# Optimization experiments

Hardware: AMD Instinct MI355X
Metric: run time of the kernel (lower is better)

## Reference

```python
import jax, jax.numpy as jnp
import numpy as np
import math

D_MODEL = 512
DIM_K = 512
DIM_V = 512
N_HEADS = 8
B, S = 2, 2048


def setup_inputs() -> dict:
    key = jax.random.key(0)
    ks = jax.random.split(key, 10)
    s = 1.0 / math.sqrt(D_MODEL)
    return {
        "x": jax.random.normal(ks[0], (B, S, D_MODEL), jnp.float32),
        "y": jax.random.normal(ks[1], (B, S, D_MODEL), jnp.float32),
        # torch nn.Linear weights: [out, in]
        "q_w": jax.random.normal(ks[2], (DIM_K, D_MODEL), jnp.float32) * s,
        "q_b": jax.random.normal(ks[3], (DIM_K,), jnp.float32) * s,
        "k_w": jax.random.normal(ks[4], (DIM_K, D_MODEL), jnp.float32) * s,
        "k_b": jax.random.normal(ks[5], (DIM_K,), jnp.float32) * s,
        "v_w": jax.random.normal(ks[6], (DIM_V, D_MODEL), jnp.float32) * s,
        "v_b": jax.random.normal(ks[7], (DIM_V,), jnp.float32) * s,
        "o_w": jax.random.normal(ks[8], (D_MODEL, DIM_V), jnp.float32) * s,
        "o_b": jax.random.normal(ks[9], (D_MODEL,), jnp.float32) * s,
    }


def reference(x, y, q_w, q_b, k_w, k_b, v_w, v_b, o_w, o_b):
    b, s, _ = x.shape
    hd_k = DIM_K // N_HEADS
    hd_v = DIM_V // N_HEADS
    norm_fact = 1.0 / math.sqrt(D_MODEL)  # note: original scales by 1/sqrt(d_model)
    # torch code reshapes the flat [B,S,dim] projection row-major into [H,B,S,hd]
    Q = (x @ q_w.T + q_b).reshape(N_HEADS, b, s, hd_k)
    K = (y @ k_w.T + k_b).reshape(N_HEADS, b, s, hd_k)
    V = (y @ v_w.T + v_b).reshape(N_HEADS, b, s, hd_v)
    # scores: [H, B, Sq, Sk]
    scores = jnp.einsum("hbqd,hbkd->hbqk", Q, K) * norm_fact
    # per-row mean threshold: mask (set -inf) where score <= row mean
    thre = jnp.mean(scores, axis=-1, keepdims=True)
    scores = jnp.where(scores <= thre, -jnp.inf, scores)
    attn = jax.nn.softmax(scores, axis=-1)
    out = jnp.einsum("hbqk,hbkd->hbqd", attn, V).reshape(b, s, DIM_V)
    return out @ o_w.T + o_b
```

## Files before the change

kernel.cpp:

```cpp
#include <hip/hip_runtime.h>


typedef unsigned short ushort;
typedef unsigned int uint;

typedef __bf16  bf16x8   __attribute__((ext_vector_type(8)));
typedef float   floatx4  __attribute__((ext_vector_type(4)));
typedef float   floatx16 __attribute__((ext_vector_type(16)));
typedef float   float4v  __attribute__((ext_vector_type(4)));
typedef uint    uint4v   __attribute__((ext_vector_type(4)));
typedef ushort  ushort4v __attribute__((ext_vector_type(4)));

#define MFMA16(a,b,c) __builtin_amdgcn_mfma_f32_16x16x32_bf16((a),(b),(c),0,0,0)
#define MFMA32(a,b,c) __builtin_amdgcn_mfma_f32_32x32x16_bf16((a),(b),(c),0,0,0)

__device__ __forceinline__ float b2f(ushort u){
  union { uint i; float f; } v; v.i = ((uint)u) << 16; return v.f;
}
__device__ __forceinline__ ushort f2b(float f){
  union { float f; uint i; } v; v.f = f;
  uint r = v.i + 0x7FFFu + ((v.i >> 16) & 1u);
  return (ushort)(r >> 16);
}
__device__ __forceinline__ void split2(float f, ushort& h, ushort& l){
  h = f2b(f);
  l = f2b(f - b2f(h));
}
__device__ __forceinline__ void gload16(const ushort* g, ushort* l){
  __builtin_amdgcn_global_load_lds(
      (const __attribute__((address_space(1))) unsigned int*)g,
      (__attribute__((address_space(3))) unsigned int*)l, 16, 0, 0);
}

__global__ __launch_bounds__(256) void split_all(
    const float* __restrict__ x, const float* __restrict__ y,
    const float* __restrict__ qw, const float* __restrict__ kw,
    const float* __restrict__ vw, const float* __restrict__ ow,
    ushort* __restrict__ xhi, ushort* __restrict__ xlo,
    ushort* __restrict__ yhi, ushort* __restrict__ ylo,
    ushort* __restrict__ qwh, ushort* __restrict__ qwl,
    ushort* __restrict__ kwh, ushort* __restrict__ kwl,
    ushort* __restrict__ vwh, ushort* __restrict__ owh)
{
  int idx = blockIdx.x * 256 + threadIdx.x;
  if (idx < 1048576){
    const float* sp; ushort *hp, *lp; int i;
    if (idx < 524288){ sp = x; hp = xhi; lp = xlo; i = idx; }
    else             { sp = y; hp = yhi; lp = ylo; i = idx - 524288; }
    float4v d = ((const float4v*)sp)[i];
    ushort4v h, l;
    #pragma unroll
    for (int j=0;j<4;j++){ ushort hh,ll; split2(d[j],hh,ll); h[j]=hh; l[j]=ll; }
    ((ushort4v*)hp)[i] = h;
    ((ushort4v*)lp)[i] = l;
  } else {
    int k = idx - 1048576;
    int a = k >> 16, i = k & 65535;
    if (a < 2){
      const float* sp = a ? kw : qw;
      ushort *hp = a ? kwh : qwh, *lp = a ? kwl : qwl;
      float4v d = ((const float4v*)sp)[i];
      ushort4v h, l;
      #pragma unroll
      for (int j=0;j<4;j++){ ushort hh,ll; split2(d[j],hh,ll); h[j]=hh; l[j]=ll; }
      ((ushort4v*)hp)[i] = h;
      ((ushort4v*)lp)[i] = l;
    } else {
      const float* sp = (a == 2) ? vw : ow;
      ushort *hp = (a == 2) ? vwh : owh;
      float4v d = ((const float4v*)sp)[i];
      ushort4v h;
      #pragma unroll
      for (int j=0;j<4;j++) h[j] = f2b(d[j]);
      ((ushort4v*)hp)[i] = h;
    }
  }
}

__global__ __launch_bounds__(256) void proj_qkv(
    const ushort* __restrict__ xhi, const ushort* __restrict__ xlo,
    const ushort* __restrict__ yhi, const ushort* __restrict__ ylo,
    const ushort* __restrict__ qwh, const ushort* __restrict__ qwl,
    const ushort* __restrict__ kwh, const ushort* __restrict__ kwl,
    const ushort* __restrict__ vwh,
    const float* __restrict__ q_b, const float* __restrict__ k_b,
    const float* __restrict__ v_b,
    ushort* __restrict__ pq_hi, ushort* __restrict__ pq_lo,
    ushort* __restrict__ pk_hi, ushort* __restrict__ pk_lo,
    ushort* __restrict__ pv, float* __restrict__ ksum_out)
{
  const int seg = blockIdx.x >> 9;
  const int id  = blockIdx.x & 511;
  const int m0 = ((id & 7) * 8 + ((id >> 3) & 7)) * 64;
  const int n0 = (id >> 6) * 64;
  const bool split = (seg < 2);

  const ushort* Ahi = (seg == 0) ? xhi : yhi;
  const ushort* Alo = (seg == 0) ? xlo : ylo;
  const ushort* Bhi = (seg == 0) ? qwh : ((seg == 1) ? kwh : vwh);
  const ushort* Blo = (seg == 0) ? qwl : kwl;
  const float*  bias = (seg == 0) ? q_b : ((seg == 1) ? k_b : v_b);
  ushort* outhi = (seg == 0) ? pq_hi : ((seg == 1) ? pk_hi : pv);
  ushort* outlo = (seg == 0) ? pq_lo : pk_lo;

  __shared__ __align__(16) ushort AH[2][4096];
  __shared__ __align__(16) ushort AL[2][4096];
  __shared__ __align__(16) ushort BH[2][4096];
  __shared__ __align__(16) ushort BL[2][4096];
  __shared__ float cs[64];

  const int t    = threadIdx.x;
  const int lane = t & 63;
  const int w    = t >> 6;
  const int wm   = w >> 1, wn = w & 1;
  const int lr   = lane & 15, lg = lane >> 4;

  const int rl  = lane >> 3;
  const int c8s = (lane & 7) ^ rl;

  auto stage = [&](int buf, int k0){
    if (split){
      #pragma unroll
      for (int j = 0; j < 8; j++){
        const int c = w * 8 + j;
        if (c < 8)
          gload16(Ahi + (size_t)(m0 + c*8 + rl)*512 + k0 + c8s*8, &AH[buf][c*512]);
        else if (c < 16)
          gload16(Alo + (size_t)(m0 + (c-8)*8 + rl)*512 + k0 + c8s*8, &AL[buf][(c-8)*512]);
        else if (c < 24)
          gload16(Bhi + (size_t)(n0 + (c-16)*8 + rl)*512 + k0 + c8s*8, &BH[buf][(c-16)*512]);
        else
          gload16(Blo + (size_t)(n0 + (c-24)*8 + rl)*512 + k0 + c8s*8, &BL[buf][(c-24)*512]);
      }
    } else {
      #pragma unroll
      for (int j = 0; j < 4; j++){
        const int c = w * 4 + j;
        if (c < 8)
          gload16(Ahi + (size_t)(m0 + c*8 + rl)*512 + k0 + c8s*8, &AH[buf][c*512]);
        else
          gload16(Bhi + (size_t)(n0 + (c-8)*8 + rl)*512 + k0 + c8s*8, &BH[buf][(c-8)*512]);
      }
    }
  };

  floatx4 zf; zf[0]=0.f; zf[1]=0.f; zf[2]=0.f; zf[3]=0.f;
  floatx4 acc[2][2];
  #pragma unroll
  for (int i=0;i<2;i++)
    #pragma unroll
    for (int j=0;j<2;j++) acc[i][j] = zf;

  stage(0, 0);
  __syncthreads();

  int cur = 0;
  for (int it = 0; it < 8; ++it){
    if (it < 7) stage(cur^1, (it+1)*64);

    #pragma unroll
    for (int ks=0; ks<2; ks++){
      const int xo = ((ks*4 + lg) ^ (lr & 7)) << 3;
      bf16x8 ah[2], al[2], bh[2], bl[2];
      #pragma unroll
      for (int mi=0;mi<2;mi++){
        const int off = (wm*32 + mi*16 + lr)*64 + xo;
        ah[mi] = *(const bf16x8*)&AH[cur][off];
        if (split) al[mi] = *(const bf16x8*)&AL[cur][off];
      }
      #pragma unroll
      for (int ni=0;ni<2;ni++){
        const int off = (wn*32 + ni*16 + lr)*64 + xo;
        bh[ni] = *(const bf16x8*)&BH[cur][off];
        if (split) bl[ni] = *(const bf16x8*)&BL[cur][off];
      }
      #pragma unroll
      for (int mi=0;mi<2;mi++)
        #pragma unroll
        for (int ni=0;ni<2;ni++){
          acc[mi][ni] = MFMA16(ah[mi], bh[ni], acc[mi][ni]);
          if (split){
            acc[mi][ni] = MFMA16(ah[mi], bl[ni], acc[mi][ni]);
            acc[mi][ni] = MFMA16(al[mi], bh[ni], acc[mi][ni]);
          }
        }
    }
    __syncthreads();
    cur ^= 1;
  }

  #pragma unroll
  for (int ni=0;ni<2;ni++){
    const int n = n0 + wn*32 + ni*16 + lr;
    const float bn = bias[n];
    #pragma unroll
    for (int mi=0;mi<2;mi++){
      #pragma unroll
      for (int r=0;r<4;r++){
        const int m = m0 + wm*32 + mi*16 + lg*4 + r;
        const float c = acc[mi][ni][r] + bn;
        const size_t off = (size_t)m*512 + n;
        if (split){ ushort h,l; split2(c,h,l); outhi[off]=h; outlo[off]=l; }
        else      { outhi[off] = f2b(c); }
      }
    }
  }

  if (seg == 1) {
    if (t < 64) cs[t] = 0.f;
    __syncthreads();
    #pragma unroll
    for (int ni=0;ni<2;ni++){
      float s = 0.f;
      #pragma unroll
      for (int mi=0;mi<2;mi++)
        #pragma unroll
        for (int r=0;r<4;r++) s += acc[mi][ni][r];
      atomicAdd(&cs[wn*32 + ni*16 + lr], s);
    }
    __syncthreads();
    if (t < 64){
      const int hb = m0 >> 8;
      atomicAdd(&ksum_out[hb*64 + t], cs[t] + 64.f * bias[n0 + t]);
    }
  }
}

__global__ __launch_bounds__(256) void vtrans(
    const ushort* __restrict__ pv, ushort* __restrict__ vt)
{
  const int hb = blockIdx.y;
  const int s0 = blockIdx.x * 64;
  const size_t cb = (size_t)hb * 131072;
  __shared__ __align__(16) ushort T[64][68];
  const int t = threadIdx.x;
  {
    int s = t >> 2, c = (t & 3) * 16;
    *(uint4v*)&T[s][c]     = *(const uint4v*)&pv[cb + (size_t)(s0+s)*64 + c];
    *(uint4v*)&T[s][c + 8] = *(const uint4v*)&pv[cb + (size_t)(s0+s)*64 + c + 8];
  }
  __syncthreads();
  const int d = t >> 2, sc = (t & 3) * 16;
  ushort buf[16];
  #pragma unroll
  for (int i=0;i<16;i++) buf[i] = T[sc + i][d];
  *(uint4v*)&vt[cb + (size_t)d*2048 + s0 + sc]     = *(const uint4v*)&buf[0];
  *(uint4v*)&vt[cb + (size_t)d*2048 + s0 + sc + 8] = *(const uint4v*)&buf[8];
}

__device__ __forceinline__ void stage_kh(
    ushort* dst, const ushort* gk, size_t cb, int kvb, int ws, int l)
{
  const int rsub = l >> 3;
  const int c8   = (l & 7) ^ rsub;
  #pragma unroll
  for (int j = 0; j < 2; j++){
    const int sub = ws*2 + j;
    const int row = sub*8 + rsub;
    gload16(gk + cb + (size_t)(kvb + row)*64 + c8*8, dst + sub*512);
  }
}
__device__ __forceinline__ void stage_vt(
    ushort* dst, const ushort* gvt, size_t cb, int kvb, int ws, int l)
{
  const int rsub = l >> 3;
  const int c8   = (l & 7) ^ rsub;
  #pragma unroll
  for (int j = 0; j < 2; j++){
    const int sub = ws*2 + j;
    const int row = sub*8 + rsub;
    gload16(gvt + cb + (size_t)row*2048 + kvb + c8*8, dst + sub*512);
  }
}

__global__ __launch_bounds__(512) void attn_kernel(
    const ushort* __restrict__ qhi, const ushort* __restrict__ qlo,
    const ushort* __restrict__ khi, const ushort* __restrict__ klo,
    const ushort* __restrict__ vt,  const float* __restrict__ ksum,
    ushort* __restrict__ Oa, ushort* __restrict__ Ob,
    float* __restrict__ za, float* __restrict__ zb)
{
  const int id = blockIdx.x;
  const int hb = ((id & 7) << 1) | ((id >> 3) & 1);
  const int kv = (id >> 4) & 1;
  const int q0 = (id >> 5) * 128;
  const size_t cb = (size_t)hb * 131072;
  const float C1 = 0.04419417382415922f * 1.44269504088896f;

  __shared__ __align__(16) ushort SMEM[32768];

  const int t = threadIdx.x, l = t & 63, w = t >> 6;
  const int half = w >> 2, ws = w & 3;
  const int lq = l & 31, h = l >> 5;
  const int kbase = kv*1024 + half*512;

  ushort* op = kv ? Ob : Oa;
  float*  zp = kv ? zb : za;

  ushort* KH0 = SMEM + (half*2)*4096;
  ushort* KH1 = SMEM + (half*2+1)*4096;
  ushort* VTB = SMEM + 16384 + half*4096;
  ushort* KLB = SMEM + 24576 + half*4096;

  stage_kh(KH0, khi, cb, kbase, ws, l);
  stage_kh(KLB, klo, cb, kbase, ws, l);

  union U8 { bf16x8 v; ushort u[8]; };
  U8 qfh[4], qfl[4];
  float part = 0.f;
  #pragma unroll
  for (int st=0; st<4; st++){
    size_t g = cb + (size_t)(q0 + ws*32 + lq)*64 + st*16 + h*8;
    qfh[st].v = *(const bf16x8*)&qhi[g];
    qfl[st].v = *(const bf16x8*)&qlo[g];
    float4v k0 = *(const float4v*)&ksum[hb*64 + st*16 + h*8];
    float4v k1 = *(const float4v*)&ksum[hb*64 + st*16 + h*8 + 4];
    #pragma unroll
    for (int j=0;j<4;j++) part += (b2f(qfh[st].u[j])   + b2f(qfl[st].u[j]))   * k0[j];
    #pragma unroll
    for (int j=0;j<4;j++) part += (b2f(qfh[st].u[4+j]) + b2f(qfl[st].u[4+j])) * k1[j];
  }
  part += __shfl_xor(part, 32);
  const float rm = part * (1.f/2048.f);
  const float nrmc = -rm * C1;

  floatx16 O0 = {0,0,0,0,0,0,0,0,0,0,0,0,0,0,0,0};
  floatx16 O1 = O0;
  float za_r = 0.f, zb_r = 0.f;

  __syncthreads();

  for (int kt = 0; kt < 8; kt++){
    ushort* KHc = (kt & 1) ? KH1 : KH0;
    ushort* KHn = (kt & 1) ? KH0 : KH1;
    if (kt + 1 < 8) stage_kh(KHn, khi, cb, kbase + (kt+1)*64, ws, l);
    stage_vt(VTB, vt, cb, kbase + kt*64, ws, l);

    floatx16 s0 = {0,0,0,0,0,0,0,0,0,0,0,0,0,0,0,0};
    floatx16 s1 = s0;
    #pragma unroll
    for (int st=0; st<4; st++){
      const int xo = (((st*2 + h) ^ (lq & 7)) << 3);
      bf16x8 kh0 = *(const bf16x8*)&KHc[(lq     )*64 + xo];
      bf16x8 kl0 = *(const bf16x8*)&KLB[(lq     )*64 + xo];
      bf16x8 kh1 = *(const bf16x8*)&KHc[(32 + lq)*64 + xo];
      bf16x8 kl1 = *(const bf16x8*)&KLB[(32 + lq)*64 + xo];
      s0 = MFMA32(kh0, qfh[st].v, s0);
      s1 = MFMA32(kh1, qfh[st].v, s1);
      s0 = MFMA32(kh0, qfl[st].v, s0);
      s1 = MFMA32(kh1, qfl[st].v, s1);
      s0 = MFMA32(kl0, qfh[st].v, s0);
      s1 = MFMA32(kl1, qfh[st].v, s1);
    }
    __syncthreads();
    if (kt + 1 < 8) stage_kh(KLB, klo, cb, kbase + (kt+1)*64, ws, l);

    #pragma unroll
    for (int r=0;r<16;r++){
      float t0 = __builtin_fmaf(s0[r], C1, nrmc);
      float t1 = __builtin_fmaf(s1[r], C1, nrmc);
      float e0 = __builtin_amdgcn_exp2f(t0);
      float e1 = __builtin_amdgcn_exp2f(t1);
      e0 = (t0 > 0.f) ? e0 : 0.f;
      e1 = (t1 > 0.f) ? e1 : 0.f;
      za_r += e0; zb_r += e1;
      s0[r] = e0; s1[r] = e1;
    }

    bf16x8 pa[4];
    #pragma unroll
    for (int g=0; g<2; g++){
      const floatx16& sp = g ? s1 : s0;
      #pragma unroll
      for (int sg=0; sg<2; sg++){
        uint X0,X1,X2,X3;
        asm("v_cvt_pk_bf16_f32 %0, %1, %2" : "=v"(X0) : "v"(sp[sg*8+0]), "v"(sp[sg*8+1]));
        asm("v_cvt_pk_bf16_f32 %0, %1, %2" : "=v"(X1) : "v"(sp[sg*8+2]), "v"(sp[sg*8+3]));
        asm("v_cvt_pk_bf16_f32 %0, %1, %2" : "=v"(X2) : "v"(sp[sg*8+4]), "v"(sp[sg*8+5]));
        asm("v_cvt_pk_bf16_f32 %0, %1, %2" : "=v"(X3) : "v"(sp[sg*8+6]), "v"(sp[sg*8+7]));
        asm("v_permlane32_swap_b32 %0, %1" : "+v"(X0), "+v"(X2));
        asm("v_permlane32_swap_b32 %0, %1" : "+v"(X1), "+v"(X3));
        union { uint u[4]; bf16x8 v; } pu;
        pu.u[0]=X0; pu.u[1]=X1; pu.u[2]=X2; pu.u[3]=X3;
        pa[g*2+sg] = pu.v;
      }
    }

    #pragma unroll
    for (int s4=0; s4<4; s4++){
      const int xo = (((s4*2 + h) ^ (lq & 7)) << 3);
      bf16x8 vf0 = *(const bf16x8*)&VTB[(lq     )*64 + xo];
      bf16x8 vf1 = *(const bf16x8*)&VTB[(32 + lq)*64 + xo];
      O0 = MFMA32(pa[s4], vf0, O0);
      O1 = MFMA32(pa[s4], vf1, O1);
    }

    __syncthreads();
  }

  float zacc = za_r + zb_r;
  zacc += __shfl_xor(zacc, 32);
  float* CB = (float*)SMEM;
  const int ci = (ws*64 + l)*34;
  if (half == 1){
    #pragma unroll
    for (int i=0;i<16;i++){ CB[ci+i] = O0[i]; CB[ci+16+i] = O1[i]; }
    CB[ci+32] = zacc;
  }
  __syncthreads();
  if (half == 0){
    const float zsum = zacc + CB[ci+32];
    if (h == 0) zp[hb*2048 + q0 + ws*32 + l] = zsum;
    #pragma unroll
    for (int r=0;r<16;r++){ O0[r] += CB[ci+r]; O1[r] += CB[ci+16+r]; }
    #pragma unroll
    for (int r=0;r<16;r++){
      const int crow = (r&3) + ((r>>2)<<3) + (h<<2);
      const int q = q0 + ws*32 + crow;
      const size_t base = cb + (size_t)q*64 + lq;
      op[base]      = f2b(O0[r]);
      op[base + 32] = f2b(O1[r]);
    }
  }
}

__global__ __launch_bounds__(256) void proj_out(
    const ushort* __restrict__ Oa, const ushort* __restrict__ Ob,
    const float* __restrict__ za, const float* __restrict__ zb,
    const ushort* __restrict__ owh, const float* __restrict__ o_b,
    float* __restrict__ outf)
{
  const int id = blockIdx.x;
  const int m0 = ((id & 7) * 8 + ((id >> 3) & 7)) * 64;
  const int n0 = (id >> 6) * 64;

  __shared__ __align__(16) ushort AH[2][4096];
  __shared__ __align__(16) ushort BH[2][4096];

  const int t    = threadIdx.x;
  const int lane = t & 63;
  const int w    = t >> 6;
  const int wm   = w >> 1, wn = w & 1;
  const int lr   = lane & 15, lg = lane >> 4;

  const int rl  = lane >> 3;
  const int c8s = (lane & 7) ^ rl;

  auto stageB = [&](int buf, int k0){
    #pragma unroll
    for (int j = 0; j < 2; j++){
      const int c = w*2 + j;
      gload16(owh + (size_t)(n0 + c*8 + rl)*512 + k0 + c8s*8, &BH[buf][c*512]);
    }
  };

  const int ar = t >> 2, ac = t & 3;
  uint4v la0, la1, lb0, lb1;
  auto issueA = [&](int k0){
    const size_t base = (size_t)(m0 + ar)*512 + k0 + ac*16;
    la0 = *(const uint4v*)&Oa[base];
    la1 = *(const uint4v*)&Oa[base + 8];
    lb0 = *(const uint4v*)&Ob[base];
    lb1 = *(const uint4v*)&Ob[base + 8];
  };
  auto writeA = [&](int buf, int k0){
    const int m = m0 + ar;
    const int zq = (m >> 8)*2048 + (m & 255)*8 + (k0 >> 6);
    const float zi = 1.f / (za[zq] + zb[zq]);
    uint4v o0, o1;
    #pragma unroll
    for (int j=0;j<4;j++){
      float l0 = (b2f((ushort)(la0[j] & 0xffff)) + b2f((ushort)(lb0[j] & 0xffff))) * zi;
      float h0 = (b2f((ushort)(la0[j] >> 16))    + b2f((ushort)(lb0[j] >> 16)))    * zi;
      o0[j] = (uint)f2b(l0) | ((uint)f2b(h0) << 16);
      float l1 = (b2f((ushort)(la1[j] & 0xffff)) + b2f((ushort)(lb1[j] & 0xffff))) * zi;
      float h1 = (b2f((ushort)(la1[j] >> 16))    + b2f((ushort)(lb1[j] >> 16)))    * zi;
      o1[j] = (uint)f2b(l1) | ((uint)f2b(h1) << 16);
    }
    const int p0 = ar*64 + (((ac*2    ) ^ (ar & 7)) << 3);
    const int p1 = ar*64 + (((ac*2 + 1) ^ (ar & 7)) << 3);
    *(uint4v*)&AH[buf][p0] = o0;
    *(uint4v*)&AH[buf][p1] = o1;
  };

  floatx4 zf; zf[0]=0.f; zf[1]=0.f; zf[2]=0.f; zf[3]=0.f;
  floatx4 acc[2][2];
  #pragma unroll
  for (int i=0;i<2;i++)
    #pragma unroll
    for (int j=0;j<2;j++) acc[i][j] = zf;

  issueA(0);
  stageB(0, 0);
  writeA(0, 0);
  __syncthreads();

  int cur = 0;
  for (int it = 0; it < 8; ++it){
    if (it < 7){ issueA((it+1)*64); stageB(cur^1, (it+1)*64); }

    #pragma unroll
    for (int ks=0; ks<2; ks++){
      const int xo = ((ks*4 + lg) ^ (lr & 7)) << 3;
      bf16x8 ah[2], bh[2];
      #pragma unroll
      for (int mi=0;mi<2;mi++)
        ah[mi] = *(const bf16x8*)&AH[cur][(wm*32 + mi*16 + lr)*64 + xo];
      #pragma unroll
      for (int ni=0;ni<2;ni++)
        bh[ni] = *(const bf16x8*)&BH[cur][(wn*32 + ni*16 + lr)*64 + xo];
      #pragma unroll
      for (int mi=0;mi<2;mi++)
        #pragma unroll
        for (int ni=0;ni<2;ni++)
          acc[mi][ni] = MFMA16(ah[mi], bh[ni], acc[mi][ni]);
    }
    if (it < 7) writeA(cur^1, (it+1)*64);
    __syncthreads();
    cur ^= 1;
  }

  #pragma unroll
  for (int ni=0;ni<2;ni++){
    const int n = n0 + wn*32 + ni*16 + lr;
    const float bn = o_b[n];
    #pragma unroll
    for (int mi=0;mi<2;mi++){
      #pragma unroll
      for (int r=0;r<4;r++){
        const int m = m0 + wm*32 + mi*16 + lg*4 + r;
        outf[(size_t)m*512 + n] = acc[mi][ni][r] + bn;
      }
    }
  }
}

extern "C" void kernel_launch(void* const* d_in, const int* in_sizes, int n_in,
                              void* d_out, int out_size, void* d_ws, size_t ws_size,
                              hipStream_t stream)
{
  const float* x   = (const float*)d_in[0];
  const float* y   = (const float*)d_in[1];
  const float* q_w = (const float*)d_in[2];
  const float* q_b = (const float*)d_in[3];
  const float* k_w = (const float*)d_in[4];
  const float* k_b = (const float*)d_in[5];
  const float* v_w = (const float*)d_in[6];
  const float* v_b = (const float*)d_in[7];
  const float* o_w = (const float*)d_in[8];
  const float* o_b = (const float*)d_in[9];

  const size_t NE = 4096ull * 512;
  const size_t WN = 512ull * 512;
  ushort* p = (ushort*)d_ws;
  ushort* pq_hi = p;
  ushort* pq_lo = pq_hi + NE;
  ushort* pk_hi = pq_lo + NE;
  ushort* pk_lo = pk_hi + NE;
  ushort* pv    = pk_lo + NE;
  ushort* xhi   = pv + NE;
  ushort* xlo   = xhi + NE;
  ushort* yhi   = xlo + NE;
  ushort* ylo   = yhi + NE;
  ushort* vtg   = xhi;
  ushort* Oa    = pv;
  ushort* Ob    = yhi;
  float*  za    = (float*)ylo;
  float*  zb    = za + 32768;
  ushort* qwh = ylo + NE;
  ushort* qwl = qwh + WN;
  ushort* kwh = qwl + WN;
  ushort* kwl = kwh + WN;
  ushort* vwh = kwl + WN;
  ushort* owh = vwh + WN;
  float*  ksumb = (float*)(owh + WN);

  hipMemsetAsync(ksumb, 0, 16 * 64 * sizeof(float), stream);

  split_all<<<5120, 256, 0, stream>>>(x, y, q_w, k_w, v_w, o_w,
                                      xhi, xlo, yhi, ylo,
                                      qwh, qwl, kwh, kwl, vwh, owh);
  proj_qkv<<<1536, 256, 0, stream>>>(xhi, xlo, yhi, ylo,
                                     qwh, qwl, kwh, kwl, vwh,
                                     q_b, k_b, v_b,
                                     pq_hi, pq_lo, pk_hi, pk_lo, pv, ksumb);
  vtrans<<<dim3(32,16), 256, 0, stream>>>(pv, vtg);
  attn_kernel<<<512, 512, 0, stream>>>(pq_hi, pq_lo, pk_hi, pk_lo, vtg, ksumb,
                                       Oa, Ob, za, zb);
  proj_out<<<512, 256, 0, stream>>>(Oa, Ob, za, zb, owh, o_b, (float*)d_out);
}
```

Baseline: 107.3 us.

## Split attention KV range four ways across smaller blocks and reduce in proj_out

The attention kernel now launches 1024 blocks of 256 threads, each handling a quarter of the key range, instead of 512 blocks of 512 threads that merged two KV halves in shared memory. The in-block shared-memory reduction goes away and proj_out instead sums four partial O and z buffers. MFMA sections are wrapped in s_setprio to favour matrix issue. This is meant to raise occupancy and remove the intra-block reduction and barrier, at the cost of twice as many bf16 partials written to global memory and more loads in proj_out. Workspace layout is reorganised to fit the four partial buffers.

```diff
diff --git a/kernel.cpp b/kernel.cpp
--- a/kernel.cpp
+++ b/kernel.cpp
@@ -249,68 +249,65 @@
 }
 
 __device__ __forceinline__ void stage_kh(
-    ushort* dst, const ushort* gk, size_t cb, int kvb, int ws, int l)
+    ushort* dst, const ushort* gk, size_t cb, int kvb, int w, int l)
 {
   const int rsub = l >> 3;
   const int c8   = (l & 7) ^ rsub;
   #pragma unroll
   for (int j = 0; j < 2; j++){
-    const int sub = ws*2 + j;
+    const int sub = w*2 + j;
     const int row = sub*8 + rsub;
     gload16(gk + cb + (size_t)(kvb + row)*64 + c8*8, dst + sub*512);
   }
 }
 __device__ __forceinline__ void stage_vt(
-    ushort* dst, const ushort* gvt, size_t cb, int kvb, int ws, int l)
+    ushort* dst, const ushort* gvt, size_t cb, int kvb, int w, int l)
 {
   const int rsub = l >> 3;
   const int c8   = (l & 7) ^ rsub;
   #pragma unroll
   for (int j = 0; j < 2; j++){
-    const int sub = ws*2 + j;
+    const int sub = w*2 + j;
     const int row = sub*8 + rsub;
     gload16(gvt + cb + (size_t)row*2048 + kvb + c8*8, dst + sub*512);
   }
 }
 
-__global__ __launch_bounds__(512) void attn_kernel(
+__global__ __launch_bounds__(256) void attn_kernel(
     const ushort* __restrict__ qhi, const ushort* __restrict__ qlo,
     const ushort* __restrict__ khi, const ushort* __restrict__ klo,
     const ushort* __restrict__ vt,  const float* __restrict__ ksum,
-    ushort* __restrict__ Oa, ushort* __restrict__ Ob,
-    float* __restrict__ za, float* __restrict__ zb)
+    ushort* __restrict__ Obase, float* __restrict__ zbase)
 {
   const int id = blockIdx.x;
   const int hb = ((id & 7) << 1) | ((id >> 3) & 1);
-  const int kv = (id >> 4) & 1;
-  const int q0 = (id >> 5) * 128;
+  const int kv = (id >> 4) & 3;
+  const int q0 = (id >> 6) * 128;
   const size_t cb = (size_t)hb * 131072;
   const float C1 = 0.04419417382415922f * 1.44269504088896f;
 
-  __shared__ __align__(16) ushort SMEM[32768];
+  __shared__ __align__(16) ushort SMEM[16384];
+  ushort* KH0 = SMEM;
+  ushort* KH1 = SMEM + 4096;
+  ushort* VTB = SMEM + 8192;
+  ushort* KLB = SMEM + 12288;
 
   const int t = threadIdx.x, l = t & 63, w = t >> 6;
-  const int half = w >> 2, ws = w & 3;
   const int lq = l & 31, h = l >> 5;
-  const int kbase = kv*1024 + half*512;
-
-  ushort* op = kv ? Ob : Oa;
-  float*  zp = kv ? zb : za;
-
-  ushort* KH0 = SMEM + (half*2)*4096;
-  ushort* KH1 = SMEM + (half*2+1)*4096;
-  ushort* VTB = SMEM + 16384 + half*4096;
-  ushort* KLB = SMEM + 24576 + half*4096;
-
-  stage_kh(KH0, khi, cb, kbase, ws, l);
-  stage_kh(KLB, klo, cb, kbase, ws, l);
+  const int kbase = kv * 512;
+
+  ushort* op = Obase + (size_t)kv * 2097152;
+  float*  zp = zbase + kv * 32768;
+
+  stage_kh(KH0, khi, cb, kbase, w, l);
+  stage_kh(KLB, klo, cb, kbase, w, l);
 
   union U8 { bf16x8 v; ushort u[8]; };
   U8 qfh[4], qfl[4];
   float part = 0.f;
   #pragma unroll
   for (int st=0; st<4; st++){
-    size_t g = cb + (size_t)(q0 + ws*32 + lq)*64 + st*16 + h*8;
+    size_t g = cb + (size_t)(q0 + w*32 + lq)*64 + st*16 + h*8;
     qfh[st].v = *(const bf16x8*)&qhi[g];
     qfl[st].v = *(const bf16x8*)&qlo[g];
     float4v k0 = *(const float4v*)&ksum[hb*64 + st*16 + h*8];
@@ -333,11 +330,12 @@
   for (int kt = 0; kt < 8; kt++){
     ushort* KHc = (kt & 1) ? KH1 : KH0;
     ushort* KHn = (kt & 1) ? KH0 : KH1;
-    if (kt + 1 < 8) stage_kh(KHn, khi, cb, kbase + (kt+1)*64, ws, l);
-    stage_vt(VTB, vt, cb, kbase + kt*64, ws, l);
+    if (kt + 1 < 8) stage_kh(KHn, khi, cb, kbase + (kt+1)*64, w, l);
+    stage_vt(VTB, vt, cb, kbase + kt*64, w, l);
 
     floatx16 s0 = {0,0,0,0,0,0,0,0,0,0,0,0,0,0,0,0};
     floatx16 s1 = s0;
+    __builtin_amdgcn_s_setprio(1);
     #pragma unroll
     for (int st=0; st<4; st++){
       const int xo = (((st*2 + h) ^ (lq & 7)) << 3);
@@ -352,8 +350,9 @@
       s0 = MFMA32(kl0, qfh[st].v, s0);
       s1 = MFMA32(kl1, qfh[st].v, s1);
     }
+    __builtin_amdgcn_s_setprio(0);
     __syncthreads();
-    if (kt + 1 < 8) stage_kh(KLB, klo, cb, kbase + (kt+1)*64, ws, l);
+    if (kt + 1 < 8) stage_kh(KLB, klo, cb, kbase + (kt+1)*64, w, l);
 
     #pragma unroll
     for (int r=0;r<16;r++){
@@ -386,6 +385,7 @@
       }
     }
 
+    __builtin_amdgcn_s_setprio(1);
     #pragma unroll
     for (int s4=0; s4<4; s4++){
       const int xo = (((s4*2 + h) ^ (lq & 7)) << 3);
@@ -394,39 +394,26 @@
       O0 = MFMA32(pa[s4], vf0, O0);
       O1 = MFMA32(pa[s4], vf1, O1);
     }
+    __builtin_amdgcn_s_setprio(0);
 
     __syncthreads();
   }
 
   float zacc = za_r + zb_r;
   zacc += __shfl_xor(zacc, 32);
-  float* CB = (float*)SMEM;
-  const int ci = (ws*64 + l)*34;
-  if (half == 1){
-    #pragma unroll
-    for (int i=0;i<16;i++){ CB[ci+i] = O0[i]; CB[ci+16+i] = O1[i]; }
-    CB[ci+32] = zacc;
-  }
-  __syncthreads();
-  if (half == 0){
-    const float zsum = zacc + CB[ci+32];
-    if (h == 0) zp[hb*2048 + q0 + ws*32 + l] = zsum;
-    #pragma unroll
-    for (int r=0;r<16;r++){ O0[r] += CB[ci+r]; O1[r] += CB[ci+16+r]; }
-    #pragma unroll
-    for (int r=0;r<16;r++){
-      const int crow = (r&3) + ((r>>2)<<3) + (h<<2);
-      const int q = q0 + ws*32 + crow;
-      const size_t base = cb + (size_t)q*64 + lq;
-      op[base]      = f2b(O0[r]);
-      op[base + 32] = f2b(O1[r]);
-    }
+  if (h == 0) zp[hb*2048 + q0 + w*32 + l] = zacc;
+  #pragma unroll
+  for (int r=0;r<16;r++){
+    const int crow = (r&3) + ((r>>2)<<3) + (h<<2);
+    const int q = q0 + w*32 + crow;
+    const size_t base = cb + (size_t)q*64 + lq;
+    op[base]      = f2b(O0[r]);
+    op[base + 32] = f2b(O1[r]);
   }
 }
 
 __global__ __launch_bounds__(256) void proj_out(
-    const ushort* __restrict__ Oa, const ushort* __restrict__ Ob,
-    const float* __restrict__ za, const float* __restrict__ zb,
+    const ushort* __restrict__ Obase, const float* __restrict__ zbase,
     const ushort* __restrict__ owh, const float* __restrict__ o_b,
     float* __restrict__ outf)
 {
@@ -455,27 +442,35 @@
   };
 
   const int ar = t >> 2, ac = t & 3;
-  uint4v la0, la1, lb0, lb1;
+  uint4v la[4][2];
   auto issueA = [&](int k0){
     const size_t base = (size_t)(m0 + ar)*512 + k0 + ac*16;
-    la0 = *(const uint4v*)&Oa[base];
-    la1 = *(const uint4v*)&Oa[base + 8];
-    lb0 = *(const uint4v*)&Ob[base];
-    lb1 = *(const uint4v*)&Ob[base + 8];
+    #pragma unroll
+    for (int p2=0;p2<4;p2++){
+      la[p2][0] = *(const uint4v*)&Obase[(size_t)p2*2097152 + base];
+      la[p2][1] = *(const uint4v*)&Obase[(size_t)p2*2097152 + base + 8];
+    }
   };
   auto writeA = [&](int buf, int k0){
     const int m = m0 + ar;
     const int zq = (m >> 8)*2048 + (m & 255)*8 + (k0 >> 6);
-    const float zi = 1.f / (za[zq] + zb[zq]);
+    float zs = 0.f;
+    #pragma unroll
+    for (int p2=0;p2<4;p2++) zs += zbase[p2*32768 + zq];
+    const float zi = 1.f / zs;
     uint4v o0, o1;
     #pragma unroll
     for (int j=0;j<4;j++){
-      float l0 = (b2f((ushort)(la0[j] & 0xffff)) + b2f((ushort)(lb0[j] & 0xffff))) * zi;
-      float h0 = (b2f((ushort)(la0[j] >> 16))    + b2f((ushort)(lb0[j] >> 16)))    * zi;
-      o0[j] = (uint)f2b(l0) | ((uint)f2b(h0) << 16);
-      float l1 = (b2f((ushort)(la1[j] & 0xffff)) + b2f((ushort)(lb1[j] & 0xffff))) * zi;
-      float h1 = (b2f((ushort)(la1[j] >> 16))    + b2f((ushort)(lb1[j] >> 16)))    * zi;
-      o1[j] = (uint)f2b(l1) | ((uint)f2b(h1) << 16);
+      float lo0=0.f, hi0=0.f, lo1=0.f, hi1=0.f;
+      #pragma unroll
+      for (int p2=0;p2<4;p2++){
+        lo0 += b2f((ushort)(la[p2][0][j] & 0xffff));
+        hi0 += b2f((ushort)(la[p2][0][j] >> 16));
+        lo1 += b2f((ushort)(la[p2][1][j] & 0xffff));
+        hi1 += b2f((ushort)(la[p2][1][j] >> 16));
+      }
+      o0[j] = (uint)f2b(lo0*zi) | ((uint)f2b(hi0*zi) << 16);
+      o1[j] = (uint)f2b(lo1*zi) | ((uint)f2b(hi1*zi) << 16);
     }
     const int p0 = ar*64 + (((ac*2    ) ^ (ar & 7)) << 3);
     const int p1 = ar*64 + (((ac*2 + 1) ^ (ar & 7)) << 3);
@@ -562,11 +557,7 @@
   ushort* xlo   = xhi + NE;
   ushort* yhi   = xlo + NE;
   ushort* ylo   = yhi + NE;
-  ushort* vtg   = xhi;
-  ushort* Oa    = pv;
-  ushort* Ob    = yhi;
-  float*  za    = (float*)ylo;
-  float*  zb    = za + 32768;
+  ushort* Obase = xhi;
   ushort* qwh = ylo + NE;
   ushort* qwl = qwh + WN;
   ushort* kwh = qwl + WN;
@@ -574,6 +565,8 @@
   ushort* vwh = kwl + WN;
   ushort* owh = vwh + WN;
   float*  ksumb = (float*)(owh + WN);
+  float*  zbase = ksumb + 1024;
+  ushort* vtg   = (ushort*)(zbase + 4*32768);
 
   hipMemsetAsync(ksumb, 0, 16 * 64 * sizeof(float), stream);
 
@@ -585,7 +578,7 @@
                                      q_b, k_b, v_b,
                                      pq_hi, pq_lo, pk_hi, pk_lo, pv, ksumb);
   vtrans<<<dim3(32,16), 256, 0, stream>>>(pv, vtg);
-  attn_kernel<<<512, 512, 0, stream>>>(pq_hi, pq_lo, pk_hi, pk_lo, vtg, ksumb,
-                                       Oa, Ob, za, zb);
-  proj_out<<<512, 256, 0, stream>>>(Oa, Ob, za, zb, owh, o_b, (float*)d_out);
-}
+  attn_kernel<<<1024, 256, 0, stream>>>(pq_hi, pq_lo, pk_hi, pk_lo, vtg, ksumb,
+                                        Obase, zbase);
+  proj_out<<<512, 256, 0, stream>>>(Obase, zbase, owh, o_b, (float*)d_out);
+}
```

After: 113.9 us. +6.1%, slower.
